# Performance work log

Measured on AMD Instinct MI355X. Metric: run time of the kernel, lower is better.

The kernel has to match this reference:

```python
import jax, jax.numpy as jnp
from jax import lax
import numpy as np
import math

B, H, W, C = 4, 32, 256, 96
EXPAND, N, R, K = 2, 16, 6, 2
DI = EXPAND * C


def setup_inputs() -> dict:
    key = jax.random.key(0)
    ks = jax.random.split(key, 10)
    x = jax.random.normal(ks[0], (B, H, W, C), jnp.float32)
    W_in = jax.random.normal(ks[1], (2 * DI, C), jnp.float32) * (C ** -0.5)
    conv_w = jax.random.normal(ks[2], (DI, 1, 3, 3), jnp.float32) * (1.0 / 3.0)
    conv_b = jnp.zeros((DI,), jnp.float32)
    x_proj_weight = jax.random.normal(ks[3], (K, R + 2 * N, DI), jnp.float32) * (DI ** -0.5)
    dt_init_std = R ** -0.5
    dt_projs_weight = jax.random.uniform(ks[4], (K, DI, R), jnp.float32, -dt_init_std, dt_init_std)
    dt_min, dt_max = 1e-3, 1e-1
    dt = jnp.exp(jax.random.uniform(ks[5], (K, DI), jnp.float32) * (math.log(dt_max) - math.log(dt_min)) + math.log(dt_min))
    dt = jnp.clip(dt, 1e-4, None)
    dt_projs_bias = dt + jnp.log(-jnp.expm1(-dt))
    A_logs = jnp.tile(jnp.log(jnp.arange(1, N + 1, dtype=jnp.float32))[None, :], (K * DI, 1))
    Ds = jnp.ones((K * DI,), jnp.float32)
    W_out = jax.random.normal(ks[6], (C, DI), jnp.float32) * (DI ** -0.5)
    return {"x": x, "W_in": W_in, "conv_w": conv_w, "conv_b": conv_b,
            "x_proj_weight": x_proj_weight, "dt_projs_weight": dt_projs_weight,
            "dt_projs_bias": dt_projs_bias, "A_logs": A_logs, "Ds": Ds, "W_out": W_out}


def reference(x, W_in, conv_w, conv_b, x_proj_weight, dt_projs_weight,
              dt_projs_bias, A_logs, Ds, W_out):
    Bb, Hh, Ww, Cc = x.shape
    DIi = conv_w.shape[0]
    Kk = x_proj_weight.shape[0]
    Nn = A_logs.shape[-1]
    Rr = dt_projs_weight.shape[-1]
    L = Hh * Ww

    # in_proj + chunk
    xz = x @ W_in.T                       # (B,H,W,2*DI)
    xc, z = xz[..., :DIi], xz[..., DIi:]
    # depthwise conv (NCHW)
    xc = jnp.transpose(xc, (0, 3, 1, 2))
    xc = lax.conv_general_dilated(xc, conv_w, (1, 1), 'SAME',
                                  dimension_numbers=('NCHW', 'OIHW', 'NCHW'),
                                  feature_group_count=DIi)
    xc = jax.nn.silu(xc + conv_b[None, :, None, None])

    # cross-scan: forward + reversed (K=2)
    xf = xc.reshape(Bb, DIi, L)
    xs = jnp.stack([xf, xf[..., ::-1]], axis=1)          # (B,K,DI,L)

    x_dbl = jnp.einsum('bkdl,kcd->bkcl', xs, x_proj_weight)
    dts_r = x_dbl[:, :, :Rr]                             # (B,K,R,L)
    Bs = x_dbl[:, :, Rr:Rr + Nn]                         # (B,K,N,L)
    Cs = x_dbl[:, :, Rr + Nn:]                           # (B,K,N,L)
    dts = jnp.einsum('bkrl,kdr->bkdl', dts_r, dt_projs_weight)

    As = -jnp.exp(A_logs).reshape(Kk, DIi, Nn)           # (K,DI,N)
    Dd = Ds.reshape(Kk, DIi)
    delta = jax.nn.softplus(dts + dt_projs_bias.reshape(1, Kk, DIi, 1))

    # sequential selective scan over L
    u_t = jnp.moveaxis(xs, -1, 0)      # (L,B,K,DI)
    d_t = jnp.moveaxis(delta, -1, 0)   # (L,B,K,DI)
    B_t = jnp.moveaxis(Bs, -1, 0)      # (L,B,K,N)
    C_t = jnp.moveaxis(Cs, -1, 0)      # (L,B,K,N)

    def step(h, inp):
        u, dlt, Bt, Ct = inp
        dA = jnp.exp(dlt[..., None] * As)                       # (B,K,DI,N)
        h = dA * h + (dlt * u)[..., None] * Bt[:, :, None, :]
        y = jnp.sum(h * Ct[:, :, None, :], axis=-1)             # (B,K,DI)
        return h, y

    h0 = jnp.zeros((Bb, Kk, DIi, Nn), x.dtype)
    _, ys = lax.scan(step, h0, (u_t, d_t, B_t, C_t))
    ys = jnp.moveaxis(ys, 0, -1)                                # (B,K,DI,L)
    ys = ys + xs * Dd[None, :, :, None]

    # un-flip reversed direction and merge
    y = ys[:, 0] + ys[:, 1][..., ::-1]                          # (B,DI,L)
    y = jnp.transpose(y.reshape(Bb, DIi, Hh, Ww), (0, 2, 3, 1)) # (B,H,W,DI)

    out = (y * jax.nn.silu(z)) @ W_out.T                        # (B,H,W,C)
    return out
```

## Files before the change

### kernel.cpp

```cpp
#include <hip/hip_runtime.h>

constexpr int Bb = 4, Hh = 32, Wd = 256, Cc = 96;
constexpr int DI = 192, Nn = 16, Rr = 6, Kk = 2;
constexpr int LL = Hh * Wd;
constexpr int ROWS = Bb * LL;
constexpr int PROJ_C = 40;
constexpr int G = 128;
constexpr int CH = LL / G;

static __device__ __forceinline__ float sigmoidf_(float v) {
  return 1.f / (1.f + __expf(-v));
}
static __device__ __forceinline__ float softplusf_(float v) {
  return v > 20.f ? v : __logf(1.f + __expf(v));
}

__global__ __launch_bounds__(256) void k_xz(const float* __restrict__ x,
                                            const float* __restrict__ Win,
                                            float* __restrict__ xc,
                                            float* __restrict__ zbuf) {
  __shared__ float xt[24][66][4];
  __shared__ float wt[24][66][4];
  const int row0 = blockIdx.x * 64;
  const int col0 = blockIdx.y * 64;
  const int tid = threadIdx.x;

  for (int idx = tid; idx < 64 * 96; idx += 256) {
    int r = idx / 96, kkk = idx % 96;
    xt[kkk >> 2][r][kkk & 3] = x[(size_t)(row0 + r) * 96 + kkk];
    wt[kkk >> 2][r][kkk & 3] = Win[(size_t)(col0 + r) * 96 + kkk];
  }
  __syncthreads();

  const int tx = tid & 15, ty = tid >> 4;
  float acc[4][4] = {};
  for (int k4 = 0; k4 < 24; ++k4) {
    float4 a4[4], b4[4];
#pragma unroll
    for (int i = 0; i < 4; ++i) {
      a4[i] = *(const float4*)&xt[k4][ty + 16 * i][0];
      b4[i] = *(const float4*)&wt[k4][tx + 16 * i][0];
    }
#pragma unroll
    for (int r = 0; r < 4; ++r)
#pragma unroll
      for (int c = 0; c < 4; ++c) {
        acc[r][c] = fmaf(a4[r].x, b4[c].x, acc[r][c]);
        acc[r][c] = fmaf(a4[r].y, b4[c].y, acc[r][c]);
        acc[r][c] = fmaf(a4[r].z, b4[c].z, acc[r][c]);
        acc[r][c] = fmaf(a4[r].w, b4[c].w, acc[r][c]);
      }
  }

#pragma unroll
  for (int r = 0; r < 4; ++r) {
    int R = row0 + ty + 16 * r;
#pragma unroll
    for (int c = 0; c < 4; ++c) {
      int col = col0 + tx + 16 * c;
      if (col < DI)
        xc[(size_t)R * DI + col] = acc[r][c];
      else
        zbuf[(size_t)R * DI + (col - DI)] = acc[r][c];
    }
  }
}

__global__ __launch_bounds__(256) void k_conv(const float* __restrict__ xc,
                                              const float* __restrict__ cw,
                                              const float* __restrict__ cbias,
                                              float* __restrict__ xf) {
  __shared__ float wl[9 * DI];
  __shared__ float bl[DI];
  const int tid = threadIdx.x;
  for (int v = tid; v < 9 * DI; v += 256) {
    int dd = v / 9, t = v % 9;
    wl[t * DI + dd] = cw[v];
  }
  if (tid < DI) bl[tid] = cbias[tid];
  __syncthreads();

  int gid = blockIdx.x * 256 + tid;
  int d4 = gid % 48;
  int rem = gid / 48;
  int w4 = rem % 64;
  int bh = rem / 64;
  int h = bh % Hh, b = bh / Hh;
  const int d0 = d4 * 4, w0 = w4 * 4;

  float4 c[3][6];
#pragma unroll
  for (int dr = 0; dr < 3; ++dr) {
    const int h2 = h + dr - 1;
    const bool hv = (unsigned)h2 < (unsigned)Hh;
    const int hc = hv ? h2 : h;
    const float* rp = xc + ((size_t)(b * LL + (hc << 8))) * DI + d0;
#pragma unroll
    for (int j = 0; j < 6; ++j) {
      const int wc = w0 - 1 + j;
      const bool wv = (unsigned)wc < (unsigned)Wd;
      const int wcc = wv ? wc : w0;
      float4 v = *(const float4*)&rp[(size_t)wcc * DI];
      const float m = (hv && wv) ? 1.f : 0.f;
      c[dr][j] = make_float4(v.x * m, v.y * m, v.z * m, v.w * m);
    }
  }

  float4 wv9[9];
#pragma unroll
  for (int t = 0; t < 9; ++t) wv9[t] = *(const float4*)&wl[t * DI + d0];
  const float4 bias4 = *(const float4*)&bl[d0];

#pragma unroll
  for (int wi = 0; wi < 4; ++wi) {
    float4 a = bias4;
#pragma unroll
    for (int dr = 0; dr < 3; ++dr)
#pragma unroll
      for (int dc = 0; dc < 3; ++dc) {
        const float4 vv = c[dr][wi + dc];
        const float4 ww = wv9[dr * 3 + dc];
        a.x = fmaf(vv.x, ww.x, a.x);
        a.y = fmaf(vv.y, ww.y, a.y);
        a.z = fmaf(vv.z, ww.z, a.z);
        a.w = fmaf(vv.w, ww.w, a.w);
      }
    float4 r;
    r.x = a.x * sigmoidf_(a.x);
    r.y = a.y * sigmoidf_(a.y);
    r.z = a.z * sigmoidf_(a.z);
    r.w = a.w * sigmoidf_(a.w);
    *(float4*)&xf[((size_t)(b * LL + (h << 8) + w0 + wi)) * DI + d0] = r;
  }
}

__global__ __launch_bounds__(256) void k_proj(const float* __restrict__ xf,
                                              const float* __restrict__ xpw,
                                              float* __restrict__ proj) {
  __shared__ float smem[5376];
  float* As = smem;
  float* Ws = smem + 32 * 68;
  const int tid = threadIdx.x;
  const int row0 = blockIdx.x * 64;
  const int b = row0 >> 13;
  const int l0 = row0 & (LL - 1);
  const int tx = tid & 15;
  const int ty = tid >> 4;
  float acc[4][5] = {};

  for (int kc = 0; kc < 6; ++kc) {
    const int d0 = kc * 32;
    __syncthreads();
    for (int v = tid; v < 512; v += 256) {
      const int l = v >> 3, dk4 = v & 7;
      const float4 xv =
          *(const float4*)&xf[((size_t)b * LL + l0 + l) * DI + d0 + dk4 * 4];
      As[(dk4 * 4 + 0) * 68 + l] = xv.x;
      As[(dk4 * 4 + 1) * 68 + l] = xv.y;
      As[(dk4 * 4 + 2) * 68 + l] = xv.z;
      As[(dk4 * 4 + 3) * 68 + l] = xv.w;
    }
    for (int v = tid; v < 640; v += 256) {
      const int s = v >> 3, dk4 = v & 7;
      const int k = s / 40, off = s % 40;
      float4 wv = make_float4(0.f, 0.f, 0.f, 0.f);
      if (off < 6 || off >= 8) {
        const int c = off < 6 ? off : off - 2;
        wv = *(const float4*)&xpw[(size_t)(k * 38 + c) * DI + d0 + dk4 * 4];
      }
      Ws[(dk4 * 4 + 0) * 84 + s] = wv.x;
      Ws[(dk4 * 4 + 1) * 84 + s] = wv.y;
      Ws[(dk4 * 4 + 2) * 84 + s] = wv.z;
      Ws[(dk4 * 4 + 3) * 84 + s] = wv.w;
    }
    __syncthreads();
    for (int dk = 0; dk < 32; ++dk) {
      const float4 a4 = *(const float4*)&As[dk * 68 + ty * 4];
      float w[5];
#pragma unroll
      for (int j = 0; j < 5; ++j) w[j] = Ws[dk * 84 + tx * 5 + j];
      const float av[4] = {a4.x, a4.y, a4.z, a4.w};
#pragma unroll
      for (int i = 0; i < 4; ++i)
#pragma unroll
        for (int j = 0; j < 5; ++j)
          acc[i][j] = fmaf(av[i], w[j], acc[i][j]);
    }
  }

  __syncthreads();
  float* res = smem;
#pragma unroll
  for (int i = 0; i < 4; ++i)
#pragma unroll
    for (int j = 0; j < 5; ++j)
      res[(ty * 4 + i) * 84 + tx * 5 + j] = acc[i][j];
  __syncthreads();
#pragma unroll
  for (int k = 0; k < 2; ++k) {
    float* dst = proj + ((size_t)(b * Kk + k) * LL + l0) * PROJ_C;
    for (int v = tid; v < 640; v += 256) {
      const int l = v / 10, q = v % 10;
      *(float4*)&dst[l * PROJ_C + q * 4] =
          *(const float4*)&res[l * 84 + k * 40 + q * 4];
    }
  }
}

__global__ __launch_bounds__(256) void k_delta(const float* __restrict__ proj,
                                               const float* __restrict__ dtw_,
                                               const float* __restrict__ dtb_,
                                               float* __restrict__ delta) {
  int gid = blockIdx.x * 256 + threadIdx.x;
  int d4 = gid % 48;
  int rem = gid / 48;
  int l = rem % LL;
  int bk = rem / LL;
  int k = bk & 1;
  const float* pr = proj + (size_t)(bk * LL + l) * PROJ_C;
  float p[6];
#pragma unroll
  for (int r = 0; r < 6; ++r) p[r] = pr[r];
  float4 res;
#pragma unroll
  for (int j = 0; j < 4; ++j) {
    int kd = k * DI + d4 * 4 + j;
    const float* w6 = dtw_ + (size_t)kd * 6;
    float draw = dtb_[kd];
#pragma unroll
    for (int r = 0; r < 6; ++r) draw = fmaf(p[r], w6[r], draw);
    ((float*)&res)[j] = softplusf_(draw);
  }
  *(float4*)&delta[(size_t)(bk * LL + l) * DI + d4 * 4] = res;
}

template <int PASS, int KD>
__global__ __launch_bounds__(256) void k_scan(
    const float* __restrict__ delta, const float* __restrict__ proj,
    const float* __restrict__ xf, const float* __restrict__ Alog,
    const float* __restrict__ Dsv, const float* __restrict__ hinit,
    float* __restrict__ hend, float* __restrict__ Pst,
    float* __restrict__ yout) {
  const int tid = threadIdx.x;
  const int sub = tid & 3, gi = tid >> 2;
  int rest = blockIdx.x;
  const int dt3 = rest % 3;  rest /= 3;
  const int g = rest % G;
  const int b = rest / G;
  const int d = dt3 * 64 + gi;
  const int kd = KD * DI + d;
  const int bk = b * Kk + KD;

  float A[4];
#pragma unroll
  for (int i = 0; i < 4; ++i) A[i] = -__expf(Alog[kd * 16 + sub * 4 + i]);

  const size_t gidx = (((size_t)(bk * G + g)) * DI + d) * Nn + sub * 4;
  float h[4];
  if (PASS == 1) {
    h[0] = h[1] = h[2] = h[3] = 0.f;
  } else {
    float4 h4 = *(const float4*)&hinit[gidx];
    h[0] = h4.x; h[1] = h4.y; h[2] = h4.z; h[3] = h4.w;
  }
  const float Dv = (PASS == 3) ? Dsv[kd] : 0.f;

  constexpr int STP = KD ? -1 : 1;
  constexpr int DSTP = STP * DI, PSTP = STP * PROJ_C;
  const int l_start = KD ? (LL - 1 - g * CH) : (g * CH);
  const float* dp = delta + ((size_t)bk * LL + l_start) * DI + d;
  const float* up = xf + ((size_t)b * LL + l_start) * DI + d;
  const float* pp = proj + ((size_t)bk * LL + l_start) * PROJ_C + 8 + sub * 4;
  const size_t ybase = ((size_t)b * DI + d) * LL;

  float dlt_c = *dp;
  float u_c = *up;
  float4 B_c = *(const float4*)pp;
  float4 C_c;
  if (PASS == 3) C_c = *(const float4*)(pp + 16);

  float dsum = 0.f, ybuf = 0.f;
#pragma unroll 4
  for (int t = 0; t < CH; ++t) {
    dp += DSTP; up += DSTP; pp += PSTP;
    const float dlt_n = *dp;
    const float u_n = *up;
    const float4 B_n = *(const float4*)pp;
    float4 C_n;
    if (PASS == 3) C_n = *(const float4*)(pp + 16);

    const float du = dlt_c * u_c;
    if (PASS == 1) {
#pragma unroll
      for (int i = 0; i < 4; ++i)
        h[i] = fmaf(__expf(dlt_c * A[i]), h[i], du * ((const float*)&B_c)[i]);
      dsum += dlt_c;
    } else {
      float yp = 0.f;
#pragma unroll
      for (int i = 0; i < 4; ++i) {
        h[i] = fmaf(__expf(dlt_c * A[i]), h[i], du * ((const float*)&B_c)[i]);
        yp = fmaf(h[i], ((const float*)&C_c)[i], yp);
      }
      yp += __shfl_xor(yp, 1, 64);
      yp += __shfl_xor(yp, 2, 64);
      const float yt = fmaf(u_c, Dv, yp);
      ybuf = ((t & 3) == sub) ? yt : ybuf;
      if ((t & 3) == 3) {
        const int tau = g * CH + (t & ~3) + sub;
        const int lp = KD ? (LL - 1 - tau) : tau;
        if (KD == 0)
          yout[ybase + lp] = ybuf;
        else
          yout[ybase + lp] += ybuf;
      }
    }
    dlt_c = dlt_n; u_c = u_n; B_c = B_n;
    if (PASS == 3) C_c = C_n;
  }
  if (PASS == 1) {
    float4 hv = make_float4(h[0], h[1], h[2], h[3]);
    float4 pv = make_float4(__expf(A[0] * dsum), __expf(A[1] * dsum),
                            __expf(A[2] * dsum), __expf(A[3] * dsum));
    *(float4*)&hend[gidx] = hv;
    *(float4*)&Pst[gidx] = pv;
  }
}

__global__ __launch_bounds__(256) void k_scan2(const float* __restrict__ hend,
                                               const float* __restrict__ Pst,
                                               float* __restrict__ hini) {
  int idx = blockIdx.x * 256 + threadIdx.x;
  int n = idx & 15;
  int rem = idx >> 4;
  int d = rem % DI;
  int bk = rem / DI;
  float carry = 0.f;
#pragma unroll 8
  for (int g = 0; g < G; ++g) {
    size_t a = (((size_t)(bk * G + g)) * DI + d) * Nn + n;
    float hv = hend[a], pv = Pst[a];
    hini[a] = carry;
    carry = fmaf(pv, carry, hv);
  }
}

__global__ __launch_bounds__(256) void k_out(const float* __restrict__ y,
                                             const float* __restrict__ zbuf,
                                             const float* __restrict__ Wout,
                                             float* __restrict__ out) {
  __shared__ float As[32][132];
  __shared__ float Ws[32][100];
  const int tid = threadIdx.x;
  const int row0 = blockIdx.x * 128;
  const int b = row0 >> 13;
  const int l0 = row0 & (LL - 1);
  const int tx = tid & 7;
  const int ty = tid >> 3;
  float acc[4][12] = {};

  for (int kc = 0; kc < 6; ++kc) {
    const int d0 = kc * 32;
    __syncthreads();
    for (int v = tid; v < 1024; v += 256) {
      const int l = v >> 3, dk4 = v & 7;
      const float4 zv = *(const float4*)&zbuf[((size_t)b * LL + l0 + l) * DI +
                                              d0 + dk4 * 4];
      As[dk4 * 4 + 0][l] = zv.x * sigmoidf_(zv.x);
      As[dk4 * 4 + 1][l] = zv.y * sigmoidf_(zv.y);
      As[dk4 * 4 + 2][l] = zv.z * sigmoidf_(zv.z);
      As[dk4 * 4 + 3][l] = zv.w * sigmoidf_(zv.w);
    }
    for (int v = tid; v < 768; v += 256) {
      const int c = v >> 3, dk4 = v & 7;
      const float4 wv = *(const float4*)&Wout[(size_t)c * DI + d0 + dk4 * 4];
      Ws[dk4 * 4 + 0][c] = wv.x;
      Ws[dk4 * 4 + 1][c] = wv.y;
      Ws[dk4 * 4 + 2][c] = wv.z;
      Ws[dk4 * 4 + 3][c] = wv.w;
    }
    __syncthreads();
    for (int v = tid; v < 1024; v += 256) {
      const int dk = v >> 5, l4 = v & 31;
      const float4 yv =
          *(const float4*)&y[((size_t)b * DI + d0 + dk) * LL + l0 + l4 * 4];
      As[dk][l4 * 4 + 0] *= yv.x;
      As[dk][l4 * 4 + 1] *= yv.y;
      As[dk][l4 * 4 + 2] *= yv.z;
      As[dk][l4 * 4 + 3] *= yv.w;
    }
    __syncthreads();
    for (int dk = 0; dk < 32; ++dk) {
      const float4 a4 = *(const float4*)&As[dk][ty * 4];
      const float4 w0 = *(const float4*)&Ws[dk][tx * 12];
      const float4 w1 = *(const float4*)&Ws[dk][tx * 12 + 4];
      const float4 w2 = *(const float4*)&Ws[dk][tx * 12 + 8];
      const float av[4] = {a4.x, a4.y, a4.z, a4.w};
      const float wv[12] = {w0.x, w0.y, w0.z, w0.w, w1.x, w1.y,
                            w1.z, w1.w, w2.x, w2.y, w2.z, w2.w};
#pragma unroll
      for (int i = 0; i < 4; ++i)
#pragma unroll
        for (int j = 0; j < 12; ++j)
          acc[i][j] = fmaf(av[i], wv[j], acc[i][j]);
    }
  }

#pragma unroll
  for (int i = 0; i < 4; ++i) {
    float* op = out + ((size_t)b * LL + l0 + ty * 4 + i) * 96 + tx * 12;
    *(float4*)(op + 0) = make_float4(acc[i][0], acc[i][1], acc[i][2], acc[i][3]);
    *(float4*)(op + 4) = make_float4(acc[i][4], acc[i][5], acc[i][6], acc[i][7]);
    *(float4*)(op + 8) = make_float4(acc[i][8], acc[i][9], acc[i][10], acc[i][11]);
  }
}

extern "C" void kernel_launch(void* const* d_in, const int* in_sizes, int n_in,
                              void* d_out, int out_size, void* d_ws,
                              size_t ws_size, hipStream_t stream) {
  const float* x    = (const float*)d_in[0];
  const float* Win  = (const float*)d_in[1];
  const float* cw   = (const float*)d_in[2];
  const float* cb   = (const float*)d_in[3];
  const float* xpw  = (const float*)d_in[4];
  const float* dtw  = (const float*)d_in[5];
  const float* dtb  = (const float*)d_in[6];
  const float* Alog = (const float*)d_in[7];
  const float* Dsv  = (const float*)d_in[8];
  const float* Wout = (const float*)d_in[9];
  float* out = (float*)d_out;

  float* ws = (float*)d_ws;
  size_t o = 0;
  float* zbuf  = ws + o;  o += (size_t)ROWS * DI;
  float* xf    = ws + o;  o += (size_t)ROWS * DI;
  float* proj  = ws + o;  o += (size_t)Bb * Kk * LL * PROJ_C;
  float* delta = ws + o;  o += (size_t)Bb * Kk * LL * DI;
  const size_t hsz = (size_t)Bb * Kk * G * DI * Nn;
  float* hend = ws + o;  o += hsz;
  float* Pst  = ws + o;  o += hsz;
  float* hini = ws + o;  o += hsz;
  float* y    = ws + o;  o += (size_t)Bb * DI * LL;
  float* xc   = y;

  k_xz<<<dim3(ROWS / 64, 6), 256, 0, stream>>>(x, Win, xc, zbuf);
  k_conv<<<dim3((Bb * Hh * 64 * 48) / 256), 256, 0, stream>>>(xc, cw, cb, xf);
  k_proj<<<dim3(ROWS / 64), 256, 0, stream>>>(xf, xpw, proj);
  k_delta<<<dim3((Bb * Kk * LL * 48) / 256), 256, 0, stream>>>(proj, dtw, dtb,
                                                               delta);
  k_scan<1, 0><<<dim3(Bb * G * 3), 256, 0, stream>>>(
      delta, proj, xf, Alog, Dsv, nullptr, hend, Pst, nullptr);
  k_scan<1, 1><<<dim3(Bb * G * 3), 256, 0, stream>>>(
      delta, proj, xf, Alog, Dsv, nullptr, hend, Pst, nullptr);
  k_scan2<<<dim3((Bb * Kk * DI * Nn) / 256), 256, 0, stream>>>(hend, Pst,
                                                               hini);
  k_scan<3, 0><<<dim3(Bb * G * 3), 256, 0, stream>>>(
      delta, proj, xf, Alog, Dsv, hini, nullptr, nullptr, y);
  k_scan<3, 1><<<dim3(Bb * G * 3), 256, 0, stream>>>(
      delta, proj, xf, Alog, Dsv, hini, nullptr, nullptr, y);
  k_out<<<dim3(ROWS / 128), 256, 0, stream>>>(y, zbuf, Wout, out);
}
```

Baseline: 356.1 us.

## Merge both scan directions into single launches and retile the in-projection GEMM

The forward and reverse scan passes now run in one launch each, with the direction taken from the block index, which doubles the grid per launch and removes two kernel launches. Each direction writes its own y buffer instead of the reverse pass doing a read-modify-write on shared y, and the output kernel sums the two buffers when it loads them. The in-projection GEMM moves to 128x96 tiles with 4x12 register blocking, K-chunked shared tiles and float4 stores. The cost is an extra y-sized buffer and one extra read stream in the output kernel.

```diff
diff --git a/kernel.cpp b/kernel.cpp
--- a/kernel.cpp
+++ b/kernel.cpp
@@ -7,6 +7,7 @@
 constexpr int PROJ_C = 40;
 constexpr int G = 128;
 constexpr int CH = LL / G;
+constexpr size_t YSZ = (size_t)Bb * DI * LL;
 
 static __device__ __forceinline__ float sigmoidf_(float v) {
   return 1.f / (1.f + __expf(-v));
@@ -19,50 +20,63 @@
                                             const float* __restrict__ Win,
                                             float* __restrict__ xc,
                                             float* __restrict__ zbuf) {
-  __shared__ float xt[24][66][4];
-  __shared__ float wt[24][66][4];
-  const int row0 = blockIdx.x * 64;
-  const int col0 = blockIdx.y * 64;
+  __shared__ float As[32][132];
+  __shared__ float Ws[32][100];
   const int tid = threadIdx.x;
-
-  for (int idx = tid; idx < 64 * 96; idx += 256) {
-    int r = idx / 96, kkk = idx % 96;
-    xt[kkk >> 2][r][kkk & 3] = x[(size_t)(row0 + r) * 96 + kkk];
-    wt[kkk >> 2][r][kkk & 3] = Win[(size_t)(col0 + r) * 96 + kkk];
-  }
-  __syncthreads();
-
-  const int tx = tid & 15, ty = tid >> 4;
-  float acc[4][4] = {};
-  for (int k4 = 0; k4 < 24; ++k4) {
-    float4 a4[4], b4[4];
-#pragma unroll
-    for (int i = 0; i < 4; ++i) {
-      a4[i] = *(const float4*)&xt[k4][ty + 16 * i][0];
-      b4[i] = *(const float4*)&wt[k4][tx + 16 * i][0];
-    }
-#pragma unroll
-    for (int r = 0; r < 4; ++r)
-#pragma unroll
-      for (int c = 0; c < 4; ++c) {
-        acc[r][c] = fmaf(a4[r].x, b4[c].x, acc[r][c]);
-        acc[r][c] = fmaf(a4[r].y, b4[c].y, acc[r][c]);
-        acc[r][c] = fmaf(a4[r].z, b4[c].z, acc[r][c]);
-        acc[r][c] = fmaf(a4[r].w, b4[c].w, acc[r][c]);
-      }
-  }
-
-#pragma unroll
-  for (int r = 0; r < 4; ++r) {
-    int R = row0 + ty + 16 * r;
-#pragma unroll
-    for (int c = 0; c < 4; ++c) {
-      int col = col0 + tx + 16 * c;
-      if (col < DI)
-        xc[(size_t)R * DI + col] = acc[r][c];
-      else
-        zbuf[(size_t)R * DI + (col - DI)] = acc[r][c];
-    }
+  const int row0 = blockIdx.x * 128;
+  const int c0 = blockIdx.y * 96;
+  const int tx = tid & 7;
+  const int ty = tid >> 3;
+  float acc[4][12] = {};
+
+  for (int kc = 0; kc < 3; ++kc) {
+    const int d0 = kc * 32;
+    __syncthreads();
+    for (int v = tid; v < 1024; v += 256) {
+      const int l = v >> 3, dk4 = v & 7;
+      const float4 xv =
+          *(const float4*)&x[(size_t)(row0 + l) * 96 + d0 + dk4 * 4];
+      As[dk4 * 4 + 0][l] = xv.x;
+      As[dk4 * 4 + 1][l] = xv.y;
+      As[dk4 * 4 + 2][l] = xv.z;
+      As[dk4 * 4 + 3][l] = xv.w;
+    }
+    for (int v = tid; v < 768; v += 256) {
+      const int c = v >> 3, dk4 = v & 7;
+      const float4 wv =
+          *(const float4*)&Win[(size_t)(c0 + c) * 96 + d0 + dk4 * 4];
+      Ws[dk4 * 4 + 0][c] = wv.x;
+      Ws[dk4 * 4 + 1][c] = wv.y;
+      Ws[dk4 * 4 + 2][c] = wv.z;
+      Ws[dk4 * 4 + 3][c] = wv.w;
+    }
+    __syncthreads();
+    for (int dk = 0; dk < 32; ++dk) {
+      const float4 a4 = *(const float4*)&As[dk][ty * 4];
+      const float4 w0 = *(const float4*)&Ws[dk][tx * 12];
+      const float4 w1 = *(const float4*)&Ws[dk][tx * 12 + 4];
+      const float4 w2 = *(const float4*)&Ws[dk][tx * 12 + 8];
+      const float av[4] = {a4.x, a4.y, a4.z, a4.w};
+      const float wv[12] = {w0.x, w0.y, w0.z, w0.w, w1.x, w1.y,
+                            w1.z, w1.w, w2.x, w2.y, w2.z, w2.w};
+#pragma unroll
+      for (int i = 0; i < 4; ++i)
+#pragma unroll
+        for (int j = 0; j < 12; ++j)
+          acc[i][j] = fmaf(av[i], wv[j], acc[i][j]);
+    }
+  }
+
+  float* dst;
+  int cc0;
+  if (c0 < DI) { dst = xc; cc0 = c0; }
+  else         { dst = zbuf; cc0 = c0 - DI; }
+#pragma unroll
+  for (int i = 0; i < 4; ++i) {
+    float* op = dst + (size_t)(row0 + ty * 4 + i) * DI + cc0 + tx * 12;
+    *(float4*)(op + 0) = make_float4(acc[i][0], acc[i][1], acc[i][2], acc[i][3]);
+    *(float4*)(op + 4) = make_float4(acc[i][4], acc[i][5], acc[i][6], acc[i][7]);
+    *(float4*)(op + 8) = make_float4(acc[i][8], acc[i][9], acc[i][10], acc[i][11]);
   }
 }
 
@@ -234,7 +248,7 @@
   *(float4*)&delta[(size_t)(bk * LL + l) * DI + d4 * 4] = res;
 }
 
-template <int PASS, int KD>
+template <int PASS>
 __global__ __launch_bounds__(256) void k_scan(
     const float* __restrict__ delta, const float* __restrict__ proj,
     const float* __restrict__ xf, const float* __restrict__ Alog,
@@ -244,12 +258,13 @@
   const int tid = threadIdx.x;
   const int sub = tid & 3, gi = tid >> 2;
   int rest = blockIdx.x;
-  const int dt3 = rest % 3;  rest /= 3;
+  const int kdir = rest & 1;  rest >>= 1;
+  const int dt3 = rest % 3;   rest /= 3;
   const int g = rest % G;
   const int b = rest / G;
   const int d = dt3 * 64 + gi;
-  const int kd = KD * DI + d;
-  const int bk = b * Kk + KD;
+  const int kd = kdir * DI + d;
+  const int bk = b * Kk + kdir;
 
   float A[4];
 #pragma unroll
@@ -265,12 +280,13 @@
   }
   const float Dv = (PASS == 3) ? Dsv[kd] : 0.f;
 
-  constexpr int STP = KD ? -1 : 1;
-  constexpr int DSTP = STP * DI, PSTP = STP * PROJ_C;
-  const int l_start = KD ? (LL - 1 - g * CH) : (g * CH);
+  const int stp = kdir ? -1 : 1;
+  const int dstp = stp * DI, pstp = stp * PROJ_C;
+  const int l_start = kdir ? (LL - 1 - g * CH) : (g * CH);
   const float* dp = delta + ((size_t)bk * LL + l_start) * DI + d;
   const float* up = xf + ((size_t)b * LL + l_start) * DI + d;
   const float* pp = proj + ((size_t)bk * LL + l_start) * PROJ_C + 8 + sub * 4;
+  float* yb = yout + (size_t)kdir * YSZ;
   const size_t ybase = ((size_t)b * DI + d) * LL;
 
   float dlt_c = *dp;
@@ -282,7 +298,7 @@
   float dsum = 0.f, ybuf = 0.f;
 #pragma unroll 4
   for (int t = 0; t < CH; ++t) {
-    dp += DSTP; up += DSTP; pp += PSTP;
+    dp += dstp; up += dstp; pp += pstp;
     const float dlt_n = *dp;
     const float u_n = *up;
     const float4 B_n = *(const float4*)pp;
@@ -308,11 +324,8 @@
       ybuf = ((t & 3) == sub) ? yt : ybuf;
       if ((t & 3) == 3) {
         const int tau = g * CH + (t & ~3) + sub;
-        const int lp = KD ? (LL - 1 - tau) : tau;
-        if (KD == 0)
-          yout[ybase + lp] = ybuf;
-        else
-          yout[ybase + lp] += ybuf;
+        const int lp = kdir ? (LL - 1 - tau) : tau;
+        yb[ybase + lp] = ybuf;
       }
     }
     dlt_c = dlt_n; u_c = u_n; B_c = B_n;
@@ -382,12 +395,13 @@
     __syncthreads();
     for (int v = tid; v < 1024; v += 256) {
       const int dk = v >> 5, l4 = v & 31;
-      const float4 yv =
-          *(const float4*)&y[((size_t)b * DI + d0 + dk) * LL + l0 + l4 * 4];
-      As[dk][l4 * 4 + 0] *= yv.x;
-      As[dk][l4 * 4 + 1] *= yv.y;
-      As[dk][l4 * 4 + 2] *= yv.z;
-      As[dk][l4 * 4 + 3] *= yv.w;
+      const size_t yi = ((size_t)b * DI + d0 + dk) * LL + l0 + l4 * 4;
+      const float4 y0v = *(const float4*)&y[yi];
+      const float4 y1v = *(const float4*)&y[YSZ + yi];
+      As[dk][l4 * 4 + 0] *= y0v.x + y1v.x;
+      As[dk][l4 * 4 + 1] *= y0v.y + y1v.y;
+      As[dk][l4 * 4 + 2] *= y0v.z + y1v.z;
+      As[dk][l4 * 4 + 3] *= y0v.w + y1v.w;
     }
     __syncthreads();
     for (int dk = 0; dk < 32; ++dk) {
@@ -440,23 +454,19 @@
   float* hend = ws + o;  o += hsz;
   float* Pst  = ws + o;  o += hsz;
   float* hini = ws + o;  o += hsz;
-  float* y    = ws + o;  o += (size_t)Bb * DI * LL;
+  float* y    = ws + o;  o += 2 * YSZ;
   float* xc   = y;
 
-  k_xz<<<dim3(ROWS / 64, 6), 256, 0, stream>>>(x, Win, xc, zbuf);
+  k_xz<<<dim3(ROWS / 128, 4), 256, 0, stream>>>(x, Win, xc, zbuf);
   k_conv<<<dim3((Bb * Hh * 64 * 48) / 256), 256, 0, stream>>>(xc, cw, cb, xf);
   k_proj<<<dim3(ROWS / 64), 256, 0, stream>>>(xf, xpw, proj);
   k_delta<<<dim3((Bb * Kk * LL * 48) / 256), 256, 0, stream>>>(proj, dtw, dtb,
                                                                delta);
-  k_scan<1, 0><<<dim3(Bb * G * 3), 256, 0, stream>>>(
-      delta, proj, xf, Alog, Dsv, nullptr, hend, Pst, nullptr);
-  k_scan<1, 1><<<dim3(Bb * G * 3), 256, 0, stream>>>(
+  k_scan<1><<<dim3(Bb * G * 3 * 2), 256, 0, stream>>>(
       delta, proj, xf, Alog, Dsv, nullptr, hend, Pst, nullptr);
   k_scan2<<<dim3((Bb * Kk * DI * Nn) / 256), 256, 0, stream>>>(hend, Pst,
                                                                hini);
-  k_scan<3, 0><<<dim3(Bb * G * 3), 256, 0, stream>>>(
-      delta, proj, xf, Alog, Dsv, hini, nullptr, nullptr, y);
-  k_scan<3, 1><<<dim3(Bb * G * 3), 256, 0, stream>>>(
+  k_scan<3><<<dim3(Bb * G * 3 * 2), 256, 0, stream>>>(
       delta, proj, xf, Alog, Dsv, hini, nullptr, nullptr, y);
   k_out<<<dim3(ROWS / 128), 256, 0, stream>>>(y, zbuf, Wout, out);
 }
```

Measured after the change: 333.7 us. -6.3%, faster.
